# Optimization experiments

Hardware: AMD Instinct MI355X
Metric: run time of the kernel (lower is better)

The kernel has to match this reference:

```python
import jax, jax.numpy as jnp
import numpy as np

N, M, D = 16384, 4096, 512
GAMMA = 1.0


def setup_inputs() -> dict:
    key = jax.random.key(0)
    kx, kc = jax.random.split(key)
    x = jax.random.normal(kx, (N, D), dtype=jnp.float32)
    centroids = jax.random.normal(kc, (M, D), dtype=jnp.float32)
    return {"x": x, "centroids": centroids}


def reference(x, centroids):
    x_sq = jnp.sum(x * x, axis=-1, keepdims=True)            # [N, 1]
    c_sq = jnp.sum(centroids * centroids, axis=-1)           # [M]
    cross = jnp.einsum('nd,md->nm', x, centroids)            # [N, M]
    dist_sq = x_sq + c_sq[None, :] - 2.0 * cross
    dist_sq = jnp.maximum(dist_sq, 0.0)  # clamp tiny negatives from fp error
    return jnp.exp(-GAMMA * dist_sq)
```

## Files before the change

kernel.cpp:

```cpp
#include <hip/hip_runtime.h>
#include <hip/hip_bf16.h>


#define NN 16384
#define MM 4096
#define DD 512

typedef float f32x4 __attribute__((ext_vector_type(4)));
typedef long i64x2 __attribute__((ext_vector_type(2)));

__device__ __forceinline__ void async16(const void* g, void* l) {
  __builtin_amdgcn_global_load_lds(
      (const __attribute__((address_space(1))) void*)g,
      (__attribute__((address_space(3))) void*)l, 16, 0, 0);
}

#define MFMA8(a, b, c) __builtin_amdgcn_mfma_f32_16x16x32_fp8_fp8(a, b, c, 0, 0, 0)
#define WAITVM(n) asm volatile("s_waitcnt vmcnt(" #n ")" ::: "memory")
#define LGKM0 asm volatile("s_waitcnt lgkmcnt(0)" ::: "memory")
#define BAR __builtin_amdgcn_s_barrier()
#define GLD4(dst, addr) \
  asm volatile("global_load_dwordx4 %0, %1, off" : "=v"(dst) : "v"(addr))
#define GLD1(dst, addr) \
  asm volatile("global_load_dword %0, %1, off" : "=v"(dst) : "v"(addr))

__global__ __launch_bounds__(256) void prep_fp8(
    const float* __restrict__ x, const float* __restrict__ c,
    unsigned char* __restrict__ x8, unsigned char* __restrict__ c8,
    float* __restrict__ xsq, float* __restrict__ csq) {
  const int w = threadIdx.x >> 6;
  const int lane = threadIdx.x & 63;
  int row = blockIdx.x * 4 + w;
  const float* src = x;
  unsigned char* dst = x8;
  float* sq = xsq;
  if (row >= NN) {
    row -= NN;
    src = c; dst = c8; sq = csq;
    if (row >= MM) return;
  }
  const float* p = src + (size_t)row * DD + lane * 8;
  float4 v0 = *(const float4*)p;
  float4 v1 = *(const float4*)(p + 4);
  float vv[8] = {v0.x, v0.y, v0.z, v0.w, v1.x, v1.y, v1.z, v1.w};
  float s = 0.f;
#pragma unroll
  for (int j = 0; j < 8; ++j) s += vv[j] * vv[j];
  int pk0 = __builtin_amdgcn_cvt_pk_fp8_f32(vv[0], vv[1], 0, false);
  int pk1 = __builtin_amdgcn_cvt_pk_fp8_f32(vv[2], vv[3], 0, false);
  int pk2 = __builtin_amdgcn_cvt_pk_fp8_f32(vv[4], vv[5], 0, false);
  int pk3 = __builtin_amdgcn_cvt_pk_fp8_f32(vv[6], vv[7], 0, false);
  uint2 wrd;
  wrd.x = (unsigned)(pk0 & 0xFFFF) | ((unsigned)pk1 << 16);
  wrd.y = (unsigned)(pk2 & 0xFFFF) | ((unsigned)pk3 << 16);
  const int db = ((lane >> 3) << 6) + ((lane & 3) << 4) + (((lane >> 2) & 1) << 3);
  *(uint2*)(dst + (size_t)row * DD + db) = wrd;
#pragma unroll
  for (int o = 32; o >= 1; o >>= 1) s += __shfl_down(s, o);
  if (lane == 0) sq[row] = s;
}

__global__ __launch_bounds__(512, 2) void rbf_gemm(
    const unsigned char* __restrict__ x8, const unsigned char* __restrict__ c8,
    const float* __restrict__ xsq, const float* __restrict__ csq,
    float* __restrict__ out) {
  __shared__ __attribute__((aligned(16))) unsigned char smem[49152];

  const int t = threadIdx.x;
  const int w = t >> 6;
  const int lane = t & 63;
  const int fr = lane & 15;
  const int fq = lane >> 4;
  const int wr = w >> 2;
  const int wc = w & 3;

  const int bid = blockIdx.x;
  const int a = bid & 7, qq = bid >> 3;
  const int x0 = ((a << 4) + (qq >> 2)) << 7;
  const int strip = qq & 3;

  const int srow = t >> 2;
  const int ssl = ((t & 3) ^ ((t >> 3) & 3)) << 4;
  const unsigned char* gx = x8 + (size_t)(x0 + srow) * DD + ssl;
  const unsigned char* gc = c8 + (size_t)srow * DD + ssl;

#define COFF(v, i)                                                   \
  ((size_t)(((((strip) << 2) + ((v) >> 3)) << 8) + (i) * 128) * DD + \
   ((v) & 7) * 64)

  const int sxor = (fq ^ ((fr >> 1) & 3)) << 4;
  const int rcb = (wc * 64 + fr) * 64 + sxor;
  const int rxb = (wr * 64 + fr) * 64 + sxor;

  f32x4 aA[4][4], aB[4][4];
  f32x4 csX[4], csY[4];
  float xsr[4];

#define MF4(AN, Q, XQ, V)                                                \
  do {                                                                   \
    _Pragma("unroll") for (int _n = 0; _n < 4; ++_n) {                   \
      f32x4 _c = ((V)&7) == 0 ? (f32x4){0.f, 0.f, 0.f, 0.f} : AN[Q][_n]; \
      _c = MFMA8(cf[_n][0], XQ[0], _c);                                  \
      AN[Q][_n] = MFMA8(cf[_n][1], XQ[1], _c);                           \
    }                                                                    \
  } while (0)

#define STFRAG4(AO, M, CSU, CPREO)                                          \
  do {                                                                      \
    const float _xn = xsr[M] * -1.4426950408889634f;                        \
    float* _orow =                                                          \
        out + (size_t)(x0 + wr * 64 + (M)*16 + fr) * MM + (CPREO) +         \
        wc * 64 + (fq << 2);                                                \
    _Pragma("unroll") for (int _n = 0; _n < 4; ++_n) {                      \
      f32x4 _v;                                                             \
      _Pragma("unroll") for (int _j = 0; _j < 4; ++_j) {                    \
        float _arg = __builtin_fmaf(                                        \
            AO[M][_n][_j], 2.8853900817779268f,                             \
            __builtin_fmaf(CSU[_n][_j], -1.4426950408889634f, _xn));        \
        _v[_j] = fminf(__builtin_exp2f(_arg), 1.0f);                        \
      }                                                                     \
      *(f32x4*)(_orow + _n * 16) = _v;                                      \
    }                                                                       \
  } while (0)

#define KT(V, AN, AO, SEN, CPREO, CSU, CSLD, CSL, CSOT, DOVM, VMN)            \
  do {                                                                       \
    const char* bX = (const char*)smem + (((V)&1) << 13);                    \
    const char* bC = (const char*)smem + 16384 + (((V)&1) << 14);            \
    char* dXw = (char*)smem + ((((V) + 1) & 1) << 13) + (w << 10);           \
    char* dCw = (char*)smem + 16384 + (((V)&1) << 14) + (w << 10);           \
    i64x2 cf[4], xqA, xqB;                                                   \
    cf[0] = *(const i64x2*)(bC + rcb);                                       \
    cf[1] = *(const i64x2*)(bC + rcb + 1024);                                \
    cf[2] = *(const i64x2*)(bC + rcb + 2048);                                \
    cf[3] = *(const i64x2*)(bC + rcb + 3072);                                \
    xqA = *(const i64x2*)(bX + rxb);                                         \
    xqB = *(const i64x2*)(bX + rxb + 1024);                                  \
    if (CSLD) {                                                              \
      const float* _cp =                                                     \
          csq + ((((strip) << 2) + (CSOT)) << 8) + wc * 64 + (fq << 2);      \
      GLD4(CSL[0], _cp); GLD4(CSL[1], _cp + 16);                             \
      GLD4(CSL[2], _cp + 32); GLD4(CSL[3], _cp + 48);                        \
    }                                                                        \
    if ((V) + 1 < 32) async16(gx + (((V) + 1) & 7) * 64, dXw);               \
    LGKM0;                                                                   \
    __builtin_amdgcn_s_setprio(1);                                           \
    MF4(AN, 0, xqA, V);                                                      \
    MF4(AN, 1, xqB, V);                                                      \
    __builtin_amdgcn_s_setprio(0);                                           \
    BAR;     \
    xqA = *(const i64x2*)(bX + rxb + 2048);                                  \
    xqB = *(const i64x2*)(bX + rxb + 3072);                                  \
    if ((V) + 2 < 32) async16(gc + COFF((V) + 2, 0), dCw);                   \
    if (SEN) STFRAG4(AO, ((V)&7) >> 1, CSU, CPREO);                          \
    if ((V) + 2 < 32) async16(gc + COFF((V) + 2, 1), dCw + 8192);            \
    LGKM0;                                                                   \
    __builtin_amdgcn_s_setprio(1);                                           \
    MF4(AN, 2, xqA, V);                                                      \
    MF4(AN, 3, xqB, V);                                                      \
    __builtin_amdgcn_s_setprio(0);                                           \
    if (DOVM) WAITVM(VMN);                                                   \
    BAR;                                                                     \
    __builtin_amdgcn_sched_barrier(0);                                       \
  } while (0)

  const int CP0 = ((strip << 2) + 0) << 8;
  const int CP1 = ((strip << 2) + 1) << 8;
  const int CP2 = ((strip << 2) + 2) << 8;
  const int CP3 = ((strip << 2) + 3) << 8;

  {
    const float* xp = xsq + x0 + wr * 64 + fr;
    GLD1(xsr[0], xp); GLD1(xsr[1], xp + 16);
    GLD1(xsr[2], xp + 32); GLD1(xsr[3], xp + 48);
  }
  async16(gc + COFF(0, 0), (char*)smem + 16384 + (w << 10));
  async16(gc + COFF(0, 1), (char*)smem + 16384 + 8192 + (w << 10));
  async16(gx, (char*)smem + (w << 10));
  async16(gc + COFF(1, 0), (char*)smem + 32768 + (w << 10));
  async16(gc + COFF(1, 1), (char*)smem + 32768 + 8192 + (w << 10));
  WAITVM(2);
  BAR;
  __builtin_amdgcn_sched_barrier(0);

  KT(0, aA, aB, 0, CP0, csX, 0, csX, 0, 1, 2);
  KT(1, aA, aB, 0, CP0, csX, 0, csX, 0, 1, 2);
  KT(2, aA, aB, 0, CP0, csX, 0, csX, 0, 1, 2);
  KT(3, aA, aB, 0, CP0, csX, 0, csX, 0, 1, 2);
  KT(4, aA, aB, 0, CP0, csX, 0, csX, 0, 1, 2);
  KT(5, aA, aB, 0, CP0, csX, 0, csX, 0, 1, 2);
  KT(6, aA, aB, 0, CP0, csX, 1, csX, 0, 1, 2);
  KT(7, aA, aB, 0, CP0, csX, 0, csX, 0, 1, 2);
  KT(8, aB, aA, 0, CP0, csX, 0, csY, 1, 1, 2);
  KT(9, aB, aA, 1, CP0, csX, 0, csY, 1, 1, 6);
  KT(10, aB, aA, 0, CP0, csX, 0, csY, 1, 1, 2);
  KT(11, aB, aA, 1, CP0, csX, 0, csY, 1, 1, 6);
  KT(12, aB, aA, 0, CP0, csX, 0, csY, 1, 1, 2);
  KT(13, aB, aA, 1, CP0, csX, 0, csY, 1, 1, 6);
  KT(14, aB, aA, 0, CP0, csX, 1, csY, 1, 1, 2);
  KT(15, aB, aA, 1, CP0, csX, 0, csY, 1, 1, 6);
  KT(16, aA, aB, 0, CP1, csY, 0, csX, 2, 1, 2);
  KT(17, aA, aB, 1, CP1, csY, 0, csX, 2, 1, 6);
  KT(18, aA, aB, 0, CP1, csY, 0, csX, 2, 1, 2);
  KT(19, aA, aB, 1, CP1, csY, 0, csX, 2, 1, 6);
  KT(20, aA, aB, 0, CP1, csY, 0, csX, 2, 1, 2);
  KT(21, aA, aB, 1, CP1, csY, 0, csX, 2, 1, 6);
  KT(22, aA, aB, 0, CP1, csY, 1, csX, 2, 1, 2);
  KT(23, aA, aB, 1, CP1, csY, 0, csX, 2, 1, 6);
  KT(24, aB, aA, 0, CP2, csX, 0, csY, 3, 1, 2);
  KT(25, aB, aA, 1, CP2, csX, 0, csY, 3, 1, 6);
  KT(26, aB, aA, 0, CP2, csX, 0, csY, 3, 1, 2);
  KT(27, aB, aA, 1, CP2, csX, 0, csY, 3, 1, 6);
  KT(28, aB, aA, 0, CP2, csX, 0, csY, 3, 1, 2);
  KT(29, aB, aA, 1, CP2, csX, 0, csY, 3, 1, 6);
  KT(30, aB, aA, 0, CP2, csX, 1, csY, 3, 1, 0);
  KT(31, aB, aA, 1, CP2, csX, 0, csY, 3, 0, 0);

  STFRAG4(aB, 0, csY, CP3);
  STFRAG4(aB, 1, csY, CP3);
  STFRAG4(aB, 2, csY, CP3);
  STFRAG4(aB, 3, csY, CP3);
}

__global__ void rbf_naive(const float* __restrict__ x,
                          const float* __restrict__ c,
                          float* __restrict__ out) {
  __shared__ float sx[16][17], sc[16][17];
  const int tx = threadIdx.x, ty = threadIdx.y;
  const int row = blockIdx.y * 16 + ty;
  const int colb = blockIdx.x * 16;
  float d = 0.f;
  for (int k0 = 0; k0 < DD; k0 += 16) {
    sx[ty][tx] = x[(size_t)row * DD + k0 + tx];
    sc[ty][tx] = c[(size_t)(colb + ty) * DD + k0 + tx];
    __syncthreads();
#pragma unroll
    for (int k = 0; k < 16; ++k) {
      float diff = sx[ty][k] - sc[tx][k];
      d += diff * diff;
    }
    __syncthreads();
  }
  out[(size_t)row * MM + colb + tx] = __expf(-d);
}

extern "C" void kernel_launch(void* const* d_in, const int* in_sizes, int n_in,
                              void* d_out, int out_size, void* d_ws,
                              size_t ws_size, hipStream_t stream) {
  const float* x = (const float*)d_in[0];
  const float* c = (const float*)d_in[1];
  float* out = (float*)d_out;

  char* ws = (char*)d_ws;
  unsigned char* x8 = (unsigned char*)ws;
  unsigned char* c8 = x8 + (size_t)NN * DD;
  float* xsq = (float*)(c8 + (size_t)MM * DD);
  float* csq = xsq + NN;
  const size_t need = (size_t)((char*)(csq + MM) - ws);

  if (ws_size < need) {
    dim3 grid(MM / 16, NN / 16), block(16, 16);
    rbf_naive<<<grid, block, 0, stream>>>(x, c, out);
    return;
  }

  prep_fp8<<<(NN + MM) / 4, 256, 0, stream>>>(x, c, x8, c8, xsq, csq);
  rbf_gemm<<<512, 512, 0, stream>>>(x8, c8, xsq, csq, out);
}
```

Before: 101.6 us.

## Double K-tile depth to 128 per stage and drop to one block per CU

Each pipeline stage now covers 128 bytes of the reduction dimension instead of 64. This halves the number of stages and barriers per output tile, and the epilogue stores are spread over every stage instead of every other one. Shared memory doubles to 96KB, launch bounds drop to one 512-thread block per CU, and the LDS swizzle widens to 8 slots to match. The trade is fewer sync points and more MFMA work per barrier, against lower occupancy and less latency hiding from a second resident block.

```diff
diff --git a/kernel.cpp b/kernel.cpp
--- a/kernel.cpp
+++ b/kernel.cpp
@@ -60,11 +60,11 @@
   if (lane == 0) sq[row] = s;
 }
 
-__global__ __launch_bounds__(512, 2) void rbf_gemm(
+__global__ __launch_bounds__(512, 1) void rbf_gemm(
     const unsigned char* __restrict__ x8, const unsigned char* __restrict__ c8,
     const float* __restrict__ xsq, const float* __restrict__ csq,
     float* __restrict__ out) {
-  __shared__ __attribute__((aligned(16))) unsigned char smem[49152];
+  __shared__ __attribute__((aligned(16))) unsigned char smem[98304];
 
   const int t = threadIdx.x;
   const int w = t >> 6;
@@ -79,30 +79,38 @@
   const int x0 = ((a << 4) + (qq >> 2)) << 7;
   const int strip = qq & 3;
 
-  const int srow = t >> 2;
-  const int ssl = ((t & 3) ^ ((t >> 3) & 3)) << 4;
+  const int srow = t >> 3;
+  const int ssl = ((t & 7) ^ ((t >> 3) & 7)) << 4;
   const unsigned char* gx = x8 + (size_t)(x0 + srow) * DD + ssl;
   const unsigned char* gc = c8 + (size_t)srow * DD + ssl;
 
+#define XOFF(v, i) ((size_t)(i)*64 * DD + ((v)&3) * 128)
 #define COFF(v, i)                                                   \
-  ((size_t)(((((strip) << 2) + ((v) >> 3)) << 8) + (i) * 128) * DD + \
-   ((v) & 7) * 64)
-
-  const int sxor = (fq ^ ((fr >> 1) & 3)) << 4;
-  const int rcb = (wc * 64 + fr) * 64 + sxor;
-  const int rxb = (wr * 64 + fr) * 64 + sxor;
+  ((size_t)(((((strip) << 2) + ((v) >> 2)) << 8) + (i)*64) * DD +    \
+   ((v)&3) * 128)
+
+  const int sxa = (fq ^ (fr & 7)) << 4;
+  const int sxb = ((fq | 4) ^ (fr & 7)) << 4;
+  const int rowC = (wc * 64 + fr) * 128;
+  const int rowX = (wr * 64 + fr) * 128;
+  const int rcb = rowC + sxa, rcbB = rowC + sxb;
+  const int rxb = rowX + sxa, rxbB = rowX + sxb;
 
   f32x4 aA[4][4], aB[4][4];
   f32x4 csX[4], csY[4];
   float xsr[4];
 
-#define MF4(AN, Q, XQ, V)                                                \
-  do {                                                                   \
-    _Pragma("unroll") for (int _n = 0; _n < 4; ++_n) {                   \
-      f32x4 _c = ((V)&7) == 0 ? (f32x4){0.f, 0.f, 0.f, 0.f} : AN[Q][_n]; \
-      _c = MFMA8(cf[_n][0], XQ[0], _c);                                  \
-      AN[Q][_n] = MFMA8(cf[_n][1], XQ[1], _c);                           \
-    }                                                                    \
+#define RD(base, off) (*(const i64x2*)((base) + (off)))
+
+#define MF16(AN, M, XA, XB, V)                                            \
+  do {                                                                    \
+    _Pragma("unroll") for (int _n = 0; _n < 4; ++_n) {                    \
+      f32x4 _c = ((V)&3) == 0 ? (f32x4){0.f, 0.f, 0.f, 0.f} : AN[M][_n];  \
+      _c = MFMA8(cfA[_n][0], XA[0], _c);                                  \
+      _c = MFMA8(cfA[_n][1], XA[1], _c);                                  \
+      _c = MFMA8(cfB[_n][0], XB[0], _c);                                  \
+      AN[M][_n] = MFMA8(cfB[_n][1], XB[1], _c);                           \
+    }                                                                     \
   } while (0)
 
 #define STFRAG4(AO, M, CSU, CPREO)                                          \
@@ -125,39 +133,46 @@
 
 #define KT(V, AN, AO, SEN, CPREO, CSU, CSLD, CSL, CSOT, DOVM, VMN)            \
   do {                                                                       \
-    const char* bX = (const char*)smem + (((V)&1) << 13);                    \
-    const char* bC = (const char*)smem + 16384 + (((V)&1) << 14);            \
-    char* dXw = (char*)smem + ((((V) + 1) & 1) << 13) + (w << 10);           \
-    char* dCw = (char*)smem + 16384 + (((V)&1) << 14) + (w << 10);           \
-    i64x2 cf[4], xqA, xqB;                                                   \
-    cf[0] = *(const i64x2*)(bC + rcb);                                       \
-    cf[1] = *(const i64x2*)(bC + rcb + 1024);                                \
-    cf[2] = *(const i64x2*)(bC + rcb + 2048);                                \
-    cf[3] = *(const i64x2*)(bC + rcb + 3072);                                \
-    xqA = *(const i64x2*)(bX + rxb);                                         \
-    xqB = *(const i64x2*)(bX + rxb + 1024);                                  \
+    const char* bX = (const char*)smem + (((V)&1) << 14);                    \
+    const char* bC = (const char*)smem + 32768 + (((V)&1) << 15);            \
+    char* dX = (char*)smem + ((((V) + 1) & 1) << 14) + (w << 10);            \
+    char* dC = (char*)smem + 32768 + (((V)&1) << 15) + (w << 10);            \
+    i64x2 cfA[4], cfB[4], xA0, xB0, xA1, xB1;                                \
     if (CSLD) {                                                              \
       const float* _cp =                                                     \
           csq + ((((strip) << 2) + (CSOT)) << 8) + wc * 64 + (fq << 2);      \
       GLD4(CSL[0], _cp); GLD4(CSL[1], _cp + 16);                             \
       GLD4(CSL[2], _cp + 32); GLD4(CSL[3], _cp + 48);                        \
     }                                                                        \
-    if ((V) + 1 < 32) async16(gx + (((V) + 1) & 7) * 64, dXw);               \
+    cfA[0] = RD(bC, rcb);          cfB[0] = RD(bC, rcbB);                    \
+    cfA[1] = RD(bC, rcb + 2048);   cfB[1] = RD(bC, rcbB + 2048);             \
+    cfA[2] = RD(bC, rcb + 4096);   cfB[2] = RD(bC, rcbB + 4096);             \
+    cfA[3] = RD(bC, rcb + 6144);   cfB[3] = RD(bC, rcbB + 6144);             \
+    xA0 = RD(bX, rxb);             xB0 = RD(bX, rxbB);                       \
+    xA1 = RD(bX, rxb + 2048);      xB1 = RD(bX, rxbB + 2048);                \
+    if ((V) + 1 < 16) {                                                      \
+      async16(gx + XOFF((V) + 1, 0), dX);                                    \
+      async16(gx + XOFF((V) + 1, 1), dX + 8192);                             \
+    }                                                                        \
     LGKM0;                                                                   \
     __builtin_amdgcn_s_setprio(1);                                           \
-    MF4(AN, 0, xqA, V);                                                      \
-    MF4(AN, 1, xqB, V);                                                      \
+    MF16(AN, 0, xA0, xB0, V);                                                \
+    MF16(AN, 1, xA1, xB1, V);                                                \
     __builtin_amdgcn_s_setprio(0);                                           \
-    BAR;     \
-    xqA = *(const i64x2*)(bX + rxb + 2048);                                  \
-    xqB = *(const i64x2*)(bX + rxb + 3072);                                  \
-    if ((V) + 2 < 32) async16(gc + COFF((V) + 2, 0), dCw);                   \
-    if (SEN) STFRAG4(AO, ((V)&7) >> 1, CSU, CPREO);                          \
-    if ((V) + 2 < 32) async16(gc + COFF((V) + 2, 1), dCw + 8192);            \
+    BAR;    \
+    xA0 = RD(bX, rxb + 4096);      xB0 = RD(bX, rxbB + 4096);                \
+    xA1 = RD(bX, rxb + 6144);      xB1 = RD(bX, rxbB + 6144);                \
+    if ((V) + 2 < 16) {                                                      \
+      async16(gc + COFF((V) + 2, 0), dC);                                    \
+      async16(gc + COFF((V) + 2, 1), dC + 8192);                             \
+      async16(gc + COFF((V) + 2, 2), dC + 16384);                            \
+      async16(gc + COFF((V) + 2, 3), dC + 24576);                            \
+    }                                                                        \
+    if (SEN) STFRAG4(AO, (V)&3, CSU, CPREO);                                 \
     LGKM0;                                                                   \
     __builtin_amdgcn_s_setprio(1);                                           \
-    MF4(AN, 2, xqA, V);                                                      \
-    MF4(AN, 3, xqB, V);                                                      \
+    MF16(AN, 2, xA0, xB0, V);                                                \
+    MF16(AN, 3, xA1, xB1, V);                                                \
     __builtin_amdgcn_s_setprio(0);                                           \
     if (DOVM) WAITVM(VMN);                                                   \
     BAR;                                                                     \
@@ -174,47 +189,36 @@
     GLD1(xsr[0], xp); GLD1(xsr[1], xp + 16);
     GLD1(xsr[2], xp + 32); GLD1(xsr[3], xp + 48);
   }
-  async16(gc + COFF(0, 0), (char*)smem + 16384 + (w << 10));
-  async16(gc + COFF(0, 1), (char*)smem + 16384 + 8192 + (w << 10));
-  async16(gx, (char*)smem + (w << 10));
-  async16(gc + COFF(1, 0), (char*)smem + 32768 + (w << 10));
-  async16(gc + COFF(1, 1), (char*)smem + 32768 + 8192 + (w << 10));
-  WAITVM(2);
+  async16(gc + COFF(0, 0), (char*)smem + 32768 + (w << 10));
+  async16(gc + COFF(0, 1), (char*)smem + 32768 + 8192 + (w << 10));
+  async16(gc + COFF(0, 2), (char*)smem + 32768 + 16384 + (w << 10));
+  async16(gc + COFF(0, 3), (char*)smem + 32768 + 24576 + (w << 10));
+  async16(gx + XOFF(0, 0), (char*)smem + (w << 10));
+  async16(gx + XOFF(0, 1), (char*)smem + 8192 + (w << 10));
+  async16(gc + COFF(1, 0), (char*)smem + 65536 + (w << 10));
+  async16(gc + COFF(1, 1), (char*)smem + 65536 + 8192 + (w << 10));
+  async16(gc + COFF(1, 2), (char*)smem + 65536 + 16384 + (w << 10));
+  async16(gc + COFF(1, 3), (char*)smem + 65536 + 24576 + (w << 10));
+  WAITVM(4);
   BAR;
   __builtin_amdgcn_sched_barrier(0);
 
-  KT(0, aA, aB, 0, CP0, csX, 0, csX, 0, 1, 2);
-  KT(1, aA, aB, 0, CP0, csX, 0, csX, 0, 1, 2);
-  KT(2, aA, aB, 0, CP0, csX, 0, csX, 0, 1, 2);
-  KT(3, aA, aB, 0, CP0, csX, 0, csX, 0, 1, 2);
-  KT(4, aA, aB, 0, CP0, csX, 0, csX, 0, 1, 2);
-  KT(5, aA, aB, 0, CP0, csX, 0, csX, 0, 1, 2);
-  KT(6, aA, aB, 0, CP0, csX, 1, csX, 0, 1, 2);
-  KT(7, aA, aB, 0, CP0, csX, 0, csX, 0, 1, 2);
-  KT(8, aB, aA, 0, CP0, csX, 0, csY, 1, 1, 2);
-  KT(9, aB, aA, 1, CP0, csX, 0, csY, 1, 1, 6);
-  KT(10, aB, aA, 0, CP0, csX, 0, csY, 1, 1, 2);
-  KT(11, aB, aA, 1, CP0, csX, 0, csY, 1, 1, 6);
-  KT(12, aB, aA, 0, CP0, csX, 0, csY, 1, 1, 2);
-  KT(13, aB, aA, 1, CP0, csX, 0, csY, 1, 1, 6);
-  KT(14, aB, aA, 0, CP0, csX, 1, csY, 1, 1, 2);
-  KT(15, aB, aA, 1, CP0, csX, 0, csY, 1, 1, 6);
-  KT(16, aA, aB, 0, CP1, csY, 0, csX, 2, 1, 2);
-  KT(17, aA, aB, 1, CP1, csY, 0, csX, 2, 1, 6);
-  KT(18, aA, aB, 0, CP1, csY, 0, csX, 2, 1, 2);
-  KT(19, aA, aB, 1, CP1, csY, 0, csX, 2, 1, 6);
-  KT(20, aA, aB, 0, CP1, csY, 0, csX, 2, 1, 2);
-  KT(21, aA, aB, 1, CP1, csY, 0, csX, 2, 1, 6);
-  KT(22, aA, aB, 0, CP1, csY, 1, csX, 2, 1, 2);
-  KT(23, aA, aB, 1, CP1, csY, 0, csX, 2, 1, 6);
-  KT(24, aB, aA, 0, CP2, csX, 0, csY, 3, 1, 2);
-  KT(25, aB, aA, 1, CP2, csX, 0, csY, 3, 1, 6);
-  KT(26, aB, aA, 0, CP2, csX, 0, csY, 3, 1, 2);
-  KT(27, aB, aA, 1, CP2, csX, 0, csY, 3, 1, 6);
-  KT(28, aB, aA, 0, CP2, csX, 0, csY, 3, 1, 2);
-  KT(29, aB, aA, 1, CP2, csX, 0, csY, 3, 1, 6);
-  KT(30, aB, aA, 0, CP2, csX, 1, csY, 3, 1, 0);
-  KT(31, aB, aA, 1, CP2, csX, 0, csY, 3, 0, 0);
+  KT(0, aA, aB, 0, CP0, csX, 0, csX, 0, 1, 4);
+  KT(1, aA, aB, 0, CP0, csX, 0, csX, 0, 1, 4);
+  KT(2, aA, aB, 0, CP0, csX, 1, csX, 0, 1, 4);
+  KT(3, aA, aB, 0, CP0, csX, 0, csX, 0, 1, 4);
+  KT(4, aB, aA, 1, CP0, csX, 0, csY, 1, 1, 8);
+  KT(5, aB, aA, 1, CP0, csX, 0, csY, 1, 1, 8);
+  KT(6, aB, aA, 1, CP0, csX, 1, csY, 1, 1, 8);
+  KT(7, aB, aA, 1, CP0, csX, 0, csY, 1, 1, 8);
+  KT(8, aA, aB, 1, CP1, csY, 0, csX, 2, 1, 8);
+  KT(9, aA, aB, 1, CP1, csY, 0, csX, 2, 1, 8);
+  KT(10, aA, aB, 1, CP1, csY, 1, csX, 2, 1, 8);
+  KT(11, aA, aB, 1, CP1, csY, 0, csX, 2, 1, 8);
+  KT(12, aB, aA, 1, CP2, csX, 0, csY, 3, 1, 8);
+  KT(13, aB, aA, 1, CP2, csX, 0, csY, 3, 1, 8);
+  KT(14, aB, aA, 1, CP2, csX, 1, csY, 3, 1, 4);
+  KT(15, aB, aA, 1, CP2, csX, 0, csY, 3, 0, 0);
 
   STFRAG4(aB, 0, csY, CP3);
   STFRAG4(aB, 1, csY, CP3);
```

New measurement: 93.29 us, median of 2. -8.1%, faster.
